# Kernel optimization log

Measured on AMD Instinct MI355X. Metric: run time of the kernel, lower is better.

The kernel has to match this reference:

```python
import jax, jax.numpy as jnp
import numpy as np

N = 100000      # num nodes
E = 1600000     # num edges
IN, HID, OUT = 256, 128, 64
ALPHA, BETA = 0.1, 1.0


def gcn_conv(x, W, b, src, dst, n):
    # PyG GCNConv: add self-loops, symmetric D^{-1/2}(A+I)D^{-1/2} normalization.
    h = x @ W  # [N, F]
    ones = jnp.ones((src.shape[0],), h.dtype)
    deg = jax.ops.segment_sum(ones, dst, num_segments=n) + 1.0  # +1 from self-loop
    dinv = jax.lax.rsqrt(deg)                                   # deg >= 1 always
    norm = dinv[src] * dinv[dst]                                # [E]
    out = jax.ops.segment_sum(norm[:, None] * h[src], dst, num_segments=n)
    out = out + (dinv * dinv)[:, None] * h                      # self-loop term
    return out + b


def group_softmax(v, seg, n):
    # torch_geometric.utils.softmax over dim 0 grouped by seg (max is detached in PyG).
    m = jax.ops.segment_max(v, seg, num_segments=n)
    num = jnp.exp(v - jax.lax.stop_gradient(m[seg]))
    den = jax.ops.segment_sum(num, seg, num_segments=n)
    return num / den[seg]


def reference(x, edge_index, edge_weight, W1, b1, W2, b2):
    src, dst = edge_index[0], edge_index[1]
    n = x.shape[0]
    h = jax.nn.relu(gcn_conv(x, W1, b1, src, dst, n))
    # F.dropout(training=False) in eval mode -> identity
    # crf_layer: per-edge scatter-add in both directions (vectorized segment_sum)
    w = (BETA * edge_weight)[:, None]  # [E,1]
    x_crf = (jax.ops.segment_sum(w * h[dst], src, num_segments=n)
             + jax.ops.segment_sum(w * h[src], dst, num_segments=n))
    # softmax(x_crf, arange(n)): each node is its own group (size 1) -> all ones.
    seg = jnp.arange(n)
    x_crf = group_softmax(x_crf, seg, n)
    h = (1.0 - ALPHA) * h + ALPHA * x_crf
    out = gcn_conv(h, W2, b2, src, dst, n)
    return jax.nn.log_softmax(out, axis=1)


def setup_inputs() -> dict:
    key = jax.random.key(0)
    k = jax.random.split(key, 6)
    x = jax.random.normal(k[0], (N, IN), jnp.float32)
    edge_index = jax.random.randint(k[1], (2, E), 0, N, dtype=jnp.int32)
    edge_weight = jnp.ones((E,), jnp.float32)
    W1 = jax.random.normal(k[2], (IN, HID), jnp.float32) * 0.05
    b1 = jnp.zeros((HID,), jnp.float32)
    W2 = jax.random.normal(k[3], (HID, OUT), jnp.float32) * 0.05
    b2 = jnp.zeros((OUT,), jnp.float32)
    return {"x": x, "edge_index": edge_index, "edge_weight": edge_weight,
            "W1": W1, "b1": b1, "W2": W2, "b2": b2}
```

## Files before the change

kernel.cpp:

```cpp
#include <hip/hip_runtime.h>
#include <math.h>


#define F_IN  256
#define F_HID 128
#define F_OUT 64
#define CSR_CAP 48
#define NBUCK 16
#define BSHIFT 13
#define BCAP  135000
#define BPAD  16

typedef __attribute__((ext_vector_type(8))) __bf16 bf16x8;
typedef __attribute__((ext_vector_type(8))) short  s16x8;
typedef __attribute__((ext_vector_type(4))) float  f32x4;

__device__ __forceinline__ unsigned short f2bf(float f) {
  unsigned u = __builtin_bit_cast(unsigned, f);
  u += 0x7fffu + ((u >> 16) & 1u);
  return (unsigned short)(u >> 16);
}
__device__ __forceinline__ float bf2f(unsigned short s) {
  unsigned u = ((unsigned)s) << 16;
  return __builtin_bit_cast(float, u);
}

__global__ void k_prep(const float* __restrict__ W1, const float* __restrict__ W2,
                       unsigned short* __restrict__ W1s, unsigned short* __restrict__ W2s,
                       int* __restrict__ zbase, int nzero) {
  const int i = blockIdx.x * 256 + threadIdx.x;
  if (i < nzero) zbase[i] = 0;
  if (i < 32768) {
    const int n = i >> 8, rem = i & 255;
    const int slot = rem >> 3, kb = rem & 7;
    const int k = ((slot ^ (n & 7)) << 3) | kb;
    W1s[i] = f2bf(W1[(size_t)k * F_HID + n]);
  } else if (i < 40960) {
    const int j = i - 32768;
    const int n = j >> 7, rem = j & 127;
    const int slot = rem >> 3, kb = rem & 7;
    const int k = ((slot ^ (n & 7)) << 3) | kb;
    W2s[j] = f2bf(W2[(size_t)k * F_OUT + n]);
  }
}

__global__ __launch_bounds__(256) void k_bin(const int* __restrict__ srcv,
                                             const int* __restrict__ dstv, int E,
                                             int* __restrict__ bcnt, uint2* __restrict__ bins) {
  __shared__ int lcnt[NBUCK];
  __shared__ int lbase[NBUCK];
  __shared__ int lpos[NBUCK];
  const int tid = threadIdx.x;
  const int per = (E + gridDim.x - 1) / gridDim.x;
  const int start = blockIdx.x * per;
  const int end = min(start + per, E);
  if (tid < NBUCK) lcnt[tid] = 0;
  __syncthreads();
  for (int e = start + tid; e < end; e += 256) {
    const int b = (int)((unsigned)dstv[e] >> BSHIFT);
    atomicAdd(&lcnt[b], 1);
  }
  __syncthreads();
  if (tid < NBUCK) {
    lbase[tid] = atomicAdd(&bcnt[tid * BPAD], lcnt[tid]);
    lpos[tid] = 0;
  }
  __syncthreads();
  for (int e = start + tid; e < end; e += 256) {
    uint2 p;
    p.x = (unsigned)srcv[e];
    p.y = (unsigned)dstv[e];
    const int b = (int)(p.y >> BSHIFT);
    const int pos = lbase[b] + atomicAdd(&lpos[b], 1);
    if (pos < BCAP) bins[(size_t)b * BCAP + pos] = p;
  }
}

__global__ __launch_bounds__(256) void k_fill_b(const uint2* __restrict__ bins,
                                                const int* __restrict__ bcnt,
                                                int* __restrict__ cnt, int* __restrict__ csr) {
  const int bucket = blockIdx.x & 15;
  const int slice = blockIdx.x >> 4;
  const int nsl = gridDim.x >> 4;
  int c = bcnt[bucket * BPAD];
  if (c > BCAP) c = BCAP;
  const uint2* bp = bins + (size_t)bucket * BCAP;
  for (int i = slice * 256 + threadIdx.x; i < c; i += nsl * 256) {
    const uint2 p = bp[i];
    const int pos = atomicAdd(&cnt[p.y], 1);
    if (pos < CSR_CAP) csr[(size_t)p.y * CSR_CAP + pos] = (int)p.x;
  }
}

__global__ void k_dinv(const int* __restrict__ cnt, float* __restrict__ dinv, int N) {
  int i = blockIdx.x * blockDim.x + threadIdx.x;
  if (i < N) dinv[i] = rsqrtf((float)cnt[i] + 1.0f);
}

__global__ __launch_bounds__(256) void k_gemm1(const float* __restrict__ X,
                                               const unsigned short* __restrict__ W1s,
                                               unsigned short* __restrict__ H, int M) {
  __shared__ unsigned short Bs[128][256];
  const int tid = threadIdx.x;
  {
    const s16x8* src = (const s16x8*)W1s;
    s16x8* dst = (s16x8*)&Bs[0][0];
#pragma unroll
    for (int i = 0; i < 16; ++i) dst[i * 256 + tid] = src[i * 256 + tid];
  }
  const int lane = tid & 63;
  const int wv_ = tid >> 6;
  const int l15 = lane & 15;
  const int kgrp = (lane >> 4) << 3;
  const int rowA = blockIdx.x * 64 + wv_ * 16 + l15;
  const int rA = rowA < M ? rowA : M - 1;
  const float* xp = &X[(size_t)rA * F_IN + kgrp];

  f32x4 acc[8];
#pragma unroll
  for (int i = 0; i < 8; ++i) acc[i] = (f32x4){0.f, 0.f, 0.f, 0.f};

  float4 a0 = *(const float4*)(xp);
  float4 a1 = *(const float4*)(xp + 4);
  __syncthreads();

#pragma unroll
  for (int k0 = 0; k0 < F_IN; k0 += 32) {
    bf16x8 af;
    {
      const float av[8] = {a0.x, a0.y, a0.z, a0.w, a1.x, a1.y, a1.z, a1.w};
#pragma unroll
      for (int j = 0; j < 8; ++j) af[j] = (__bf16)av[j];
    }
    if (k0 + 32 < F_IN) {
      a0 = *(const float4*)(xp + k0 + 32);
      a1 = *(const float4*)(xp + k0 + 36);
    }
    const int kc = (k0 + kgrp) >> 3;
#pragma unroll
    for (int nf = 0; nf < 8; ++nf) {
      const int n = nf * 16 + l15;
      const s16x8 braw = *(const s16x8*)&Bs[n][(kc ^ (n & 7)) << 3];
      const bf16x8 bv = __builtin_bit_cast(bf16x8, braw);
      acc[nf] = __builtin_amdgcn_mfma_f32_16x16x32_bf16(af, bv, acc[nf], 0, 0, 0);
    }
  }
  const int rowD = blockIdx.x * 64 + wv_ * 16 + ((lane >> 4) << 2);
#pragma unroll
  for (int r = 0; r < 4; ++r) {
    if (rowD + r < M) {
      unsigned short* hp = &H[(size_t)(rowD + r) * F_HID + l15];
#pragma unroll
      for (int nf = 0; nf < 8; ++nf) hp[nf * 16] = f2bf(acc[nf][r]);
    }
  }
}

__global__ __launch_bounds__(256) void k_gemm2(const unsigned short* __restrict__ A1,
                                               const unsigned short* __restrict__ W2s,
                                               unsigned short* __restrict__ H2, int M) {
  __shared__ unsigned short Bs[64][128];
  const int tid = threadIdx.x;
  {
    const s16x8* src = (const s16x8*)W2s;
    s16x8* dst = (s16x8*)&Bs[0][0];
#pragma unroll
    for (int i = 0; i < 4; ++i) dst[i * 256 + tid] = src[i * 256 + tid];
  }
  const int lane = tid & 63;
  const int wv_ = tid >> 6;
  const int l15 = lane & 15;
  const int kgrp = (lane >> 4) << 3;
  const int rowA = blockIdx.x * 64 + wv_ * 16 + l15;
  const int rA = rowA < M ? rowA : M - 1;
  const unsigned short* ap = &A1[(size_t)rA * F_HID + kgrp];

  f32x4 acc[4];
#pragma unroll
  for (int i = 0; i < 4; ++i) acc[i] = (f32x4){0.f, 0.f, 0.f, 0.f};

  s16x8 raw = *(const s16x8*)(ap);
  __syncthreads();

#pragma unroll
  for (int k0 = 0; k0 < F_HID; k0 += 32) {
    bf16x8 af;
#pragma unroll
    for (int j = 0; j < 8; ++j) {
      float f = bf2f((unsigned short)raw[j]);
      f = 0.9f * fmaxf(f, 0.0f) + 0.1f;
      af[j] = (__bf16)f;
    }
    if (k0 + 32 < F_HID) raw = *(const s16x8*)(ap + k0 + 32);
    const int kc = (k0 + kgrp) >> 3;
#pragma unroll
    for (int nf = 0; nf < 4; ++nf) {
      const int n = nf * 16 + l15;
      const s16x8 braw = *(const s16x8*)&Bs[n][(kc ^ (n & 7)) << 3];
      const bf16x8 bv = __builtin_bit_cast(bf16x8, braw);
      acc[nf] = __builtin_amdgcn_mfma_f32_16x16x32_bf16(af, bv, acc[nf], 0, 0, 0);
    }
  }
  const int rowD = blockIdx.x * 64 + wv_ * 16 + ((lane >> 4) << 2);
#pragma unroll
  for (int r = 0; r < 4; ++r) {
    if (rowD + r < M) {
      unsigned short* hp = &H2[(size_t)(rowD + r) * F_OUT + l15];
#pragma unroll
      for (int nf = 0; nf < 4; ++nf) hp[nf * 16] = f2bf(acc[nf][r]);
    }
  }
}

__global__ __launch_bounds__(256) void k_gather1(const int* __restrict__ cnt,
                                                 const int* __restrict__ csr,
                                                 const float* __restrict__ dinv,
                                                 const unsigned short* __restrict__ h0,
                                                 const float* __restrict__ b1,
                                                 unsigned short* __restrict__ agg1, int N) {
  const int node = (blockIdx.x << 2) + (threadIdx.x >> 6);
  if (node >= N) return;
  const int lane = threadIdx.x & 63;
  int d_ = cnt[node];
  if (d_ > CSR_CAP) d_ = CSR_CAP;
  const int* cp = &csr[(size_t)node * CSR_CAP];
  const float dv = dinv[node];
  const unsigned self = *(const unsigned*)&h0[(size_t)node * F_HID + lane * 2];
  const float2 bb = *(const float2*)&b1[lane * 2];
  float ax = dv * dv * bf2f((unsigned short)(self & 0xffff)) + bb.x;
  float ay = dv * dv * bf2f((unsigned short)(self >> 16)) + bb.y;
  int j = 0;
  for (; j + 3 < d_; j += 4) {
    const int s0 = cp[j], s1 = cp[j + 1], s2 = cp[j + 2], s3 = cp[j + 3];
    const float w0 = dinv[s0] * dv, w1 = dinv[s1] * dv, w2 = dinv[s2] * dv, w3 = dinv[s3] * dv;
    const unsigned v0 = *(const unsigned*)&h0[(size_t)s0 * F_HID + lane * 2];
    const unsigned v1 = *(const unsigned*)&h0[(size_t)s1 * F_HID + lane * 2];
    const unsigned v2 = *(const unsigned*)&h0[(size_t)s2 * F_HID + lane * 2];
    const unsigned v3 = *(const unsigned*)&h0[(size_t)s3 * F_HID + lane * 2];
    ax += w0 * bf2f((unsigned short)(v0 & 0xffff)) + w1 * bf2f((unsigned short)(v1 & 0xffff))
        + w2 * bf2f((unsigned short)(v2 & 0xffff)) + w3 * bf2f((unsigned short)(v3 & 0xffff));
    ay += w0 * bf2f((unsigned short)(v0 >> 16)) + w1 * bf2f((unsigned short)(v1 >> 16))
        + w2 * bf2f((unsigned short)(v2 >> 16)) + w3 * bf2f((unsigned short)(v3 >> 16));
  }
  for (; j < d_; ++j) {
    const int s = cp[j];
    const float w = dinv[s] * dv;
    const unsigned v = *(const unsigned*)&h0[(size_t)s * F_HID + lane * 2];
    ax += w * bf2f((unsigned short)(v & 0xffff));
    ay += w * bf2f((unsigned short)(v >> 16));
  }
  const unsigned packed = (unsigned)f2bf(ax) | ((unsigned)f2bf(ay) << 16);
  *(unsigned*)&agg1[(size_t)node * F_HID + lane * 2] = packed;
}

__global__ __launch_bounds__(256) void k_gather2_lsm(const int* __restrict__ cnt,
                                                     const int* __restrict__ csr,
                                                     const float* __restrict__ dinv,
                                                     const unsigned short* __restrict__ h2,
                                                     const float* __restrict__ b2,
                                                     float* __restrict__ outv, int N) {
  const int node = (blockIdx.x << 2) + (threadIdx.x >> 6);
  if (node >= N) return;
  const int lane = threadIdx.x & 63;
  int d_ = cnt[node];
  if (d_ > CSR_CAP) d_ = CSR_CAP;
  const int* cp = &csr[(size_t)node * CSR_CAP];
  const float dv = dinv[node];
  float acc = dv * dv * bf2f(h2[(size_t)node * F_OUT + lane]) + b2[lane];
  int j = 0;
  for (; j + 3 < d_; j += 4) {
    const int s0 = cp[j], s1 = cp[j + 1], s2 = cp[j + 2], s3 = cp[j + 3];
    const float p0 = dinv[s0] * bf2f(h2[(size_t)s0 * F_OUT + lane]);
    const float p1 = dinv[s1] * bf2f(h2[(size_t)s1 * F_OUT + lane]);
    const float p2 = dinv[s2] * bf2f(h2[(size_t)s2 * F_OUT + lane]);
    const float p3 = dinv[s3] * bf2f(h2[(size_t)s3 * F_OUT + lane]);
    acc += dv * (p0 + p1 + p2 + p3);
  }
  for (; j < d_; ++j) {
    const int s = cp[j];
    acc += dinv[s] * dv * bf2f(h2[(size_t)s * F_OUT + lane]);
  }
  float m = acc;
#pragma unroll
  for (int off = 32; off; off >>= 1) m = fmaxf(m, __shfl_xor(m, off));
  const float ex = expf(acc - m);
  float s = ex;
#pragma unroll
  for (int off = 32; off; off >>= 1) s += __shfl_xor(s, off);
  outv[(size_t)node * F_OUT + lane] = acc - m - logf(s);
}

extern "C" void kernel_launch(void* const* d_in, const int* in_sizes, int n_in,
                              void* d_out, int out_size, void* d_ws, size_t ws_size,
                              hipStream_t stream) {
  const float* x  = (const float*)d_in[0];
  const int*   ei = (const int*)d_in[1];
  const float* W1 = (const float*)d_in[3];
  const float* b1 = (const float*)d_in[4];
  const float* W2 = (const float*)d_in[5];
  const float* b2 = (const float*)d_in[6];

  const int N = in_sizes[0] / F_IN;
  const int E = in_sizes[1] / 2;
  const int* srcv = ei;
  const int* dstv = ei + E;

  float* ws = (float*)d_ws;
  const size_t Na = ((size_t)N + 511) & ~(size_t)255;
  int* bcnt = (int*)ws;
  int* cnt  = bcnt + NBUCK * BPAD;
  float* dinv = ws + Na;
  unsigned short* W1s = (unsigned short*)(ws + 2 * Na);
  unsigned short* W2s = (unsigned short*)(ws + 2 * Na + 16384);
  int* csr = (int*)(ws + 2 * Na + 16384 + 4096);
  size_t off = 2 * Na + 16384 + 4096 + (((size_t)N * CSR_CAP + 255) & ~(size_t)255);
  unsigned short* h2b   = (unsigned short*)(ws + off);
  off += ((size_t)N * (F_OUT / 2) + 255) & ~(size_t)255;
  unsigned short* agg1b = (unsigned short*)(ws + off);
  off += ((size_t)N * (F_HID / 2) + 255) & ~(size_t)255;
  unsigned short* h0b   = (unsigned short*)(ws + off);
  uint2* bins = (uint2*)h0b;
  float* outp = (float*)d_out;

  const int nzero = N + NBUCK * BPAD;
  const int prep_grid = (max(nzero, 40960) + 255) / 256;
  k_prep<<<prep_grid, 256, 0, stream>>>(W1, W2, W1s, W2s, bcnt, nzero);
  k_bin<<<512, 256, 0, stream>>>(srcv, dstv, E, bcnt, bins);
  k_fill_b<<<1024, 256, 0, stream>>>(bins, bcnt, cnt, csr);
  k_dinv<<<(N + 255) / 256, 256, 0, stream>>>(cnt, dinv, N);

  k_gemm1<<<(N + 63) / 64, 256, 0, stream>>>(x, W1s, h0b, N);
  k_gather1<<<(N + 3) / 4, 256, 0, stream>>>(cnt, csr, dinv, h0b, b1, agg1b, N);

  k_gemm2<<<(N + 63) / 64, 256, 0, stream>>>(agg1b, W2s, h2b, N);
  k_gather2_lsm<<<(N + 3) / 4, 256, 0, stream>>>(cnt, csr, dinv, h2b, b2, outp, N);
}
```

Before: 453.1 us.

## Split neighbor gathers across quarter-wavefronts with wide loads and shuffle reduction

Both gather kernels now load the node's CSR neighbor indices and weights cooperatively, one per lane, and broadcast them with shuffles. Each 16-lane quarter of the wavefront handles a different neighbor using 16-byte (or 8-byte) vector row loads, and the partial sums are combined with xor shuffles at the end. This gives more loads in flight with fewer, wider memory transactions and removes the serial per-lane index/dinv loads. The cost is extra cross-lane reduction work, and the log-softmax reduction is rewritten over 16 lanes with 4 values per lane.

New measurement: 427.7 us. 1.06x faster.

```diff
diff --git a/kernel.cpp b/kernel.cpp
--- a/kernel.cpp
+++ b/kernel.cpp
@@ -13,6 +13,7 @@
 
 typedef __attribute__((ext_vector_type(8))) __bf16 bf16x8;
 typedef __attribute__((ext_vector_type(8))) short  s16x8;
+typedef __attribute__((ext_vector_type(4))) short  s16x4;
 typedef __attribute__((ext_vector_type(4))) float  f32x4;
 
 __device__ __forceinline__ unsigned short f2bf(float f) {
@@ -221,36 +222,45 @@
   const int node = (blockIdx.x << 2) + (threadIdx.x >> 6);
   if (node >= N) return;
   const int lane = threadIdx.x & 63;
+  const int grp = lane >> 4;
+  const int l15 = lane & 15;
   int d_ = cnt[node];
   if (d_ > CSR_CAP) d_ = CSR_CAP;
-  const int* cp = &csr[(size_t)node * CSR_CAP];
   const float dv = dinv[node];
-  const unsigned self = *(const unsigned*)&h0[(size_t)node * F_HID + lane * 2];
-  const float2 bb = *(const float2*)&b1[lane * 2];
-  float ax = dv * dv * bf2f((unsigned short)(self & 0xffff)) + bb.x;
-  float ay = dv * dv * bf2f((unsigned short)(self >> 16)) + bb.y;
-  int j = 0;
-  for (; j + 3 < d_; j += 4) {
-    const int s0 = cp[j], s1 = cp[j + 1], s2 = cp[j + 2], s3 = cp[j + 3];
-    const float w0 = dinv[s0] * dv, w1 = dinv[s1] * dv, w2 = dinv[s2] * dv, w3 = dinv[s3] * dv;
-    const unsigned v0 = *(const unsigned*)&h0[(size_t)s0 * F_HID + lane * 2];
-    const unsigned v1 = *(const unsigned*)&h0[(size_t)s1 * F_HID + lane * 2];
-    const unsigned v2 = *(const unsigned*)&h0[(size_t)s2 * F_HID + lane * 2];
-    const unsigned v3 = *(const unsigned*)&h0[(size_t)s3 * F_HID + lane * 2];
-    ax += w0 * bf2f((unsigned short)(v0 & 0xffff)) + w1 * bf2f((unsigned short)(v1 & 0xffff))
-        + w2 * bf2f((unsigned short)(v2 & 0xffff)) + w3 * bf2f((unsigned short)(v3 & 0xffff));
-    ay += w0 * bf2f((unsigned short)(v0 >> 16)) + w1 * bf2f((unsigned short)(v1 >> 16))
-        + w2 * bf2f((unsigned short)(v2 >> 16)) + w3 * bf2f((unsigned short)(v3 >> 16));
-  }
-  for (; j < d_; ++j) {
-    const int s = cp[j];
-    const float w = dinv[s] * dv;
-    const unsigned v = *(const unsigned*)&h0[(size_t)s * F_HID + lane * 2];
-    ax += w * bf2f((unsigned short)(v & 0xffff));
-    ay += w * bf2f((unsigned short)(v >> 16));
-  }
-  const unsigned packed = (unsigned)f2bf(ax) | ((unsigned)f2bf(ay) << 16);
-  *(unsigned*)&agg1[(size_t)node * F_HID + lane * 2] = packed;
+  int mysrc = 0;
+  float myw = 0.f;
+  if (lane < d_) {
+    mysrc = csr[(size_t)node * CSR_CAP + lane];
+    myw = dinv[mysrc] * dv;
+  }
+  float acc[8] = {0.f, 0.f, 0.f, 0.f, 0.f, 0.f, 0.f, 0.f};
+  const int nq = (d_ + 3) >> 2;
+#pragma unroll 2
+  for (int q = 0; q < nq; ++q) {
+    const int idx = (q << 2) + grp;
+    const int s = __shfl(mysrc, idx);
+    const float w = __shfl(myw, idx);
+    const s16x8 v = *(const s16x8*)&h0[(size_t)s * F_HID + l15 * 8];
+#pragma unroll
+    for (int i = 0; i < 8; ++i) acc[i] += w * bf2f((unsigned short)v[i]);
+  }
+#pragma unroll
+  for (int i = 0; i < 8; ++i) {
+    acc[i] += __shfl_xor(acc[i], 16);
+    acc[i] += __shfl_xor(acc[i], 32);
+  }
+  if (grp == 0) {
+    const s16x8 sv = *(const s16x8*)&h0[(size_t)node * F_HID + l15 * 8];
+    const float4 bb0 = *(const float4*)&b1[l15 * 8];
+    const float4 bb1 = *(const float4*)&b1[l15 * 8 + 4];
+    const float bl[8] = {bb0.x, bb0.y, bb0.z, bb0.w, bb1.x, bb1.y, bb1.z, bb1.w};
+    const float d2 = dv * dv;
+    s16x8 o;
+#pragma unroll
+    for (int i = 0; i < 8; ++i)
+      o[i] = (short)f2bf(acc[i] + d2 * bf2f((unsigned short)sv[i]) + bl[i]);
+    *(s16x8*)&agg1[(size_t)node * F_HID + l15 * 8] = o;
+  }
 }
 
 __global__ __launch_bounds__(256) void k_gather2_lsm(const int* __restrict__ cnt,
@@ -262,32 +272,53 @@
   const int node = (blockIdx.x << 2) + (threadIdx.x >> 6);
   if (node >= N) return;
   const int lane = threadIdx.x & 63;
+  const int grp = lane >> 4;
+  const int l15 = lane & 15;
   int d_ = cnt[node];
   if (d_ > CSR_CAP) d_ = CSR_CAP;
-  const int* cp = &csr[(size_t)node * CSR_CAP];
   const float dv = dinv[node];
-  float acc = dv * dv * bf2f(h2[(size_t)node * F_OUT + lane]) + b2[lane];
-  int j = 0;
-  for (; j + 3 < d_; j += 4) {
-    const int s0 = cp[j], s1 = cp[j + 1], s2 = cp[j + 2], s3 = cp[j + 3];
-    const float p0 = dinv[s0] * bf2f(h2[(size_t)s0 * F_OUT + lane]);
-    const float p1 = dinv[s1] * bf2f(h2[(size_t)s1 * F_OUT + lane]);
-    const float p2 = dinv[s2] * bf2f(h2[(size_t)s2 * F_OUT + lane]);
-    const float p3 = dinv[s3] * bf2f(h2[(size_t)s3 * F_OUT + lane]);
-    acc += dv * (p0 + p1 + p2 + p3);
-  }
-  for (; j < d_; ++j) {
-    const int s = cp[j];
-    acc += dinv[s] * dv * bf2f(h2[(size_t)s * F_OUT + lane]);
-  }
-  float m = acc;
-#pragma unroll
-  for (int off = 32; off; off >>= 1) m = fmaxf(m, __shfl_xor(m, off));
-  const float ex = expf(acc - m);
-  float s = ex;
-#pragma unroll
-  for (int off = 32; off; off >>= 1) s += __shfl_xor(s, off);
-  outv[(size_t)node * F_OUT + lane] = acc - m - logf(s);
+  int mysrc = 0;
+  float myw = 0.f;
+  if (lane < d_) {
+    mysrc = csr[(size_t)node * CSR_CAP + lane];
+    myw = dinv[mysrc] * dv;
+  }
+  float acc[4] = {0.f, 0.f, 0.f, 0.f};
+  const int nq = (d_ + 3) >> 2;
+#pragma unroll 2
+  for (int q = 0; q < nq; ++q) {
+    const int idx = (q << 2) + grp;
+    const int s = __shfl(mysrc, idx);
+    const float w = __shfl(myw, idx);
+    const s16x4 v = *(const s16x4*)&h2[(size_t)s * F_OUT + l15 * 4];
+#pragma unroll
+    for (int i = 0; i < 4; ++i) acc[i] += w * bf2f((unsigned short)v[i]);
+  }
+#pragma unroll
+  for (int i = 0; i < 4; ++i) {
+    acc[i] += __shfl_xor(acc[i], 16);
+    acc[i] += __shfl_xor(acc[i], 32);
+  }
+  const s16x4 sv = *(const s16x4*)&h2[(size_t)node * F_OUT + l15 * 4];
+  const float4 bb = *(const float4*)&b2[l15 * 4];
+  const float bl[4] = {bb.x, bb.y, bb.z, bb.w};
+  const float d2 = dv * dv;
+  float lg[4];
+#pragma unroll
+  for (int i = 0; i < 4; ++i) lg[i] = acc[i] + d2 * bf2f((unsigned short)sv[i]) + bl[i];
+  float m = fmaxf(fmaxf(lg[0], lg[1]), fmaxf(lg[2], lg[3]));
+#pragma unroll
+  for (int off = 1; off < 16; off <<= 1) m = fmaxf(m, __shfl_xor(m, off));
+  float s = 0.f;
+#pragma unroll
+  for (int i = 0; i < 4; ++i) s += expf(lg[i] - m);
+#pragma unroll
+  for (int off = 1; off < 16; off <<= 1) s += __shfl_xor(s, off);
+  const float lse = m + logf(s);
+  if (grp == 0) {
+    float4 o = {lg[0] - lse, lg[1] - lse, lg[2] - lse, lg[3] - lse};
+    *(float4*)&outv[(size_t)node * F_OUT + l15 * 4] = o;
+  }
 }
 
 extern "C" void kernel_launch(void* const* d_in, const int* in_sizes, int n_in,
```
